# Performance work log

Hardware: AMD Instinct MI355X
Metric: run time of the kernel (lower is better)

## Reference

```python
import jax, jax.numpy as jnp
import numpy as np

N, E, D = 100000, 640000, 128

def setup_inputs() -> dict:
    key = jax.random.key(0)
    ks = jax.random.split(key, 12)
    s = 1.0 / np.sqrt(D)
    sg = 1.0 / np.sqrt(2 * D)
    return {
        "nodes": jax.random.normal(ks[0], (N, D), jnp.float32),
        "globals_": jax.random.normal(ks[1], (1, D), jnp.float32),
        "senders": jax.random.randint(ks[2], (E,), 0, N, jnp.int32),
        "receivers": jax.random.randint(ks[3], (E,), 0, N, jnp.int32),
        "W1_w": jax.random.normal(ks[4], (D, D), jnp.float32) * s,
        "W1_b": jnp.zeros((D,), jnp.float32),
        "W2_w": jax.random.normal(ks[5], (D, D), jnp.float32) * s,
        "W2_b": jnp.zeros((D,), jnp.float32),
        "W3_w": jax.random.normal(ks[6], (D, D), jnp.float32) * s,
        "W3_b": jnp.zeros((D,), jnp.float32),
        "Wg_w": jax.random.normal(ks[7], (2 * D, D), jnp.float32) * sg,
        "Wg_b": jnp.zeros((D,), jnp.float32),
    }


def reference(nodes, globals_, senders, receivers,
              W1_w, W1_b, W2_w, W2_b, W3_w, W3_b, Wg_w, Wg_b):
    n = nodes.shape[0]
    # W1 skip-branch projection
    h = nodes @ W1_w + W1_b                              # [N, D]
    # GraphConvolution: W2 projection + symmetric-normalized sum aggregation
    conv = nodes @ W2_w + W2_b                           # [N, D]
    ones = jnp.ones(senders.shape, conv.dtype)
    send_deg = jax.ops.segment_sum(ones, senders, num_segments=n)
    recv_deg = jax.ops.segment_sum(ones, receivers, num_segments=n)
    conv = conv * jax.lax.rsqrt(jnp.maximum(send_deg, 1.0))[:, None]
    agg = jax.ops.segment_sum(conv[senders], receivers, num_segments=n)  # gather + scatter
    agg = agg * jax.lax.rsqrt(jnp.maximum(recv_deg, 1.0))[:, None]
    h = h + agg
    # global -> node broadcast (globals is not None)
    h = h + (globals_[0:1] @ W3_w + W3_b)
    h = jax.nn.relu(h)
    h = h + nodes                                        # residual
    # global update: aggregate nodes (sum over single graph) + gated residual
    an = jnp.sum(h, axis=0, keepdims=True)               # [1, D]
    g_new = globals_ + jax.nn.relu(jnp.concatenate([an, globals_], axis=-1) @ Wg_w + Wg_b)
    return h, g_new
```

## Files before the change

kernel.cpp:

```cpp
#include <hip/hip_runtime.h>

#define D 128

typedef __attribute__((ext_vector_type(8))) short short8;
typedef __attribute__((ext_vector_type(4))) float floatx4;

__device__ inline void bf16split(float x, ushort& hi, ushort& lo) {
  unsigned u = __float_as_uint(x);
  unsigned rh = (u + 0x7FFFu + ((u >> 16) & 1u)) & 0xFFFF0000u;
  hi = (ushort)(rh >> 16);
  float fl = x - __uint_as_float(rh);
  unsigned ul = __float_as_uint(fl);
  lo = (ushort)((ul + 0x7FFFu + ((ul >> 16) & 1u)) >> 16);
}

__global__ void k_gproj(const float* __restrict__ g, const float* __restrict__ W3,
                        const float* __restrict__ b3, float* __restrict__ gvec) {
  const int j = threadIdx.x;
  float acc = b3[j];
  for (int k = 0; k < D; ++k) acc = fmaf(g[k], W3[k * D + j], acc);
  gvec[j] = acc;
}

__global__ void k_degrees(const int* __restrict__ snd, const int* __restrict__ rcv,
                          int* __restrict__ cs, int* __restrict__ cr, int E) {
  const int e = blockIdx.x * blockDim.x + threadIdx.x;
  if (e < E) {
    atomicAdd(cs + snd[e], 1);
    atomicAdd(cr + rcv[e], 1);
  }
}

__global__ void k_scan(const int* __restrict__ cnt, int* __restrict__ off,
                       int* __restrict__ cursor, int n) {
  __shared__ int part[1024];
  const int t = threadIdx.x;
  int s = 0;
  for (int r = t; r < n; r += 1024) s += cnt[r];
  part[t] = s;
  __syncthreads();
  for (int st = 1; st < 1024; st <<= 1) {
    int v = (t >= st) ? part[t - st] : 0;
    __syncthreads();
    part[t] += v;
    __syncthreads();
  }
  int running = (t == 0) ? 0 : part[t - 1];
  for (int r = t; r < n; r += 1024) {
    off[r] = running;
    cursor[r] = running;
    running += cnt[r];
  }
}

__global__ void k_fill(const int* __restrict__ snd, const int* __restrict__ rcv,
                       int* __restrict__ cursor, int* __restrict__ srt, int E) {
  const int e = blockIdx.x * blockDim.x + threadIdx.x;
  if (e < E) {
    const int p = atomicAdd(cursor + rcv[e], 1);
    srt[p] = snd[e];
  }
}

__global__ void k_wsplit(const float* __restrict__ W1, const float* __restrict__ W2,
                         ushort* __restrict__ wt) {
  const int id = blockIdx.x * blockDim.x + threadIdx.x;
  const int mat = id >> 14;
  const int idx = id & 16383;
  const int k = idx >> 7;
  const int n = idx & 127;
  const float x = (mat ? W2 : W1)[k * D + n];
  ushort hi, lo;
  bf16split(x, hi, lo);
  wt[(size_t)mat * 32768 + (size_t)n * 128 + k] = hi;
  wt[(size_t)mat * 32768 + 16384 + (size_t)n * 128 + k] = lo;
}

__global__ __launch_bounds__(256, 2) void k_dualgemm(
    const float* __restrict__ A, const ushort* __restrict__ wt,
    const float* __restrict__ b1, const float* __restrict__ b2,
    const float* __restrict__ gvec, const int* __restrict__ cnt_send,
    float* __restrict__ outH, float* __restrict__ conv, int n) {
  __shared__ ushort Ah[128 * 64], Al[128 * 64], Wh[128 * 64], Wl[128 * 64];
  const int t = threadIdx.x;
  const int variant = blockIdx.y;
  const int row0 = blockIdx.x * 128;
  const int lane = t & 63, widx = t >> 6;
  const int wr = widx >> 1, wc = widx & 1;
  const int m = lane & 15, quad = lane >> 4;
  const ushort* wtb = wt + (size_t)variant * 32768;

  floatx4 acc[4][4];
#pragma unroll
  for (int i = 0; i < 4; ++i)
#pragma unroll
    for (int j = 0; j < 4; ++j) acc[i][j] = (floatx4)0.f;

  const int srow = t >> 1, shalf = t & 1;

  for (int p = 0; p < 2; ++p) {
    {
      const int grow = row0 + srow;
      const bool ok = grow < n;
      const float* gp = A + (size_t)grow * D + p * 64 + shalf * 32;
#pragma unroll
      for (int c = 0; c < 8; ++c) {
        float4 v = make_float4(0.f, 0.f, 0.f, 0.f);
        if (ok) v = *(const float4*)(gp + 4 * c);
        ushort h0, l0, h1, l1, h2, l2, h3, l3;
        bf16split(v.x, h0, l0); bf16split(v.y, h1, l1);
        bf16split(v.z, h2, l2); bf16split(v.w, h3, l3);
        const int kl = shalf * 32 + 4 * c;
        const int ch = (kl >> 3) ^ (srow & 7);
        const int a = srow * 64 + ch * 8 + (kl & 7);
        *(ushort4*)&Ah[a] = make_ushort4(h0, h1, h2, h3);
        *(ushort4*)&Al[a] = make_ushort4(l0, l1, l2, l3);
      }
    }
    {
      const ushort* gh = wtb + (size_t)srow * 128 + p * 64 + shalf * 32;
      const ushort* gl = gh + 16384;
#pragma unroll
      for (int c = 0; c < 4; ++c) {
        const uint4 vh = *(const uint4*)(gh + 8 * c);
        const uint4 vl = *(const uint4*)(gl + 8 * c);
        const int ch = (shalf * 4 + c) ^ (srow & 7);
        const int a = srow * 64 + ch * 8;
        *(uint4*)&Wh[a] = vh;
        *(uint4*)&Wl[a] = vl;
      }
    }
    __syncthreads();
#pragma unroll
    for (int kk = 0; kk < 2; ++kk) {
      const int swz = (((kk << 2) + quad) ^ (lane & 7)) << 3;
      short8 a_h[4], a_l[4], b_h[4], b_l[4];
#pragma unroll
      for (int i = 0; i < 4; ++i) {
        const int r = (wr * 64 + i * 16 + m) * 64 + swz;
        a_h[i] = *(const short8*)&Ah[r];
        a_l[i] = *(const short8*)&Al[r];
      }
#pragma unroll
      for (int j = 0; j < 4; ++j) {
        const int r = (wc * 64 + j * 16 + m) * 64 + swz;
        b_h[j] = *(const short8*)&Wh[r];
        b_l[j] = *(const short8*)&Wl[r];
      }
#pragma unroll
      for (int i = 0; i < 4; ++i)
#pragma unroll
        for (int j = 0; j < 4; ++j) {
          floatx4 c = acc[i][j];
          c = __builtin_amdgcn_mfma_f32_16x16x32_bf16(a_h[i], b_h[j], c, 0, 0, 0);
          c = __builtin_amdgcn_mfma_f32_16x16x32_bf16(a_h[i], b_l[j], c, 0, 0, 0);
          c = __builtin_amdgcn_mfma_f32_16x16x32_bf16(a_l[i], b_h[j], c, 0, 0, 0);
          acc[i][j] = c;
        }
    }
    __syncthreads();
  }

  if (variant == 0) {
    float bb[4], gg[4];
#pragma unroll
    for (int j = 0; j < 4; ++j) {
      const int col = wc * 64 + j * 16 + m;
      bb[j] = b1[col];
      gg[j] = gvec[col];
    }
#pragma unroll
    for (int i = 0; i < 4; ++i)
#pragma unroll
      for (int pp = 0; pp < 4; ++pp) {
        const int rg = row0 + wr * 64 + i * 16 + quad * 4 + pp;
        if (rg >= n) continue;
#pragma unroll
        for (int j = 0; j < 4; ++j) {
          const int col = wc * 64 + j * 16 + m;
          outH[(size_t)rg * D + col] = acc[i][j][pp] + bb[j] + gg[j];
        }
      }
  } else {
    float bb[4];
#pragma unroll
    for (int j = 0; j < 4; ++j) bb[j] = b2[wc * 64 + j * 16 + m];
#pragma unroll
    for (int i = 0; i < 4; ++i)
#pragma unroll
      for (int pp = 0; pp < 4; ++pp) {
        const int rg = row0 + wr * 64 + i * 16 + quad * 4 + pp;
        if (rg >= n) continue;
        const float sc = rsqrtf(fmaxf((float)cnt_send[rg], 1.f));
#pragma unroll
        for (int j = 0; j < 4; ++j) {
          const int col = wc * 64 + j * 16 + m;
          conv[(size_t)rg * D + col] = (acc[i][j][pp] + bb[j]) * sc;
        }
      }
  }
}

__global__ __launch_bounds__(256) void k_agg_finalize(
    const float* __restrict__ conv, const int* __restrict__ off,
    const int* __restrict__ cnt_recv, const int* __restrict__ srt,
    const float* __restrict__ nodes, float* __restrict__ h,
    float* __restrict__ an, int n) {
  __shared__ float anl[8][D];
  const int hw = threadIdx.x >> 5;
  const int ln = threadIdx.x & 31;
  const int ghw = blockIdx.x * 8 + hw;
  const int nhw = gridDim.x * 8;
  const int c0 = ln * 4;

  float a0 = 0.f, a1 = 0.f, a2 = 0.f, a3 = 0.f;
  for (int r = ghw; r < n; r += nhw) {
    const int dg = cnt_recv[r];
    const int o = off[r];
    const float4 h1 = *(const float4*)(h + (size_t)r * D + c0);
    const float4 nd = *(const float4*)(nodes + (size_t)r * D + c0);
    float sx = 0.f, sy = 0.f, sz = 0.f, sw = 0.f;
    for (int i = 0; i < dg; i += 8) {
      int idx[8];
      float mk[8];
#pragma unroll
      for (int j = 0; j < 8; ++j) {
        const int p = i + j;
        const bool v = p < dg;
        idx[j] = srt[o + (v ? p : 0)];
        mk[j] = v ? 1.f : 0.f;
      }
      float4 c[8];
#pragma unroll
      for (int j = 0; j < 8; ++j)
        c[j] = *(const float4*)(conv + (size_t)idx[j] * D + c0);
#pragma unroll
      for (int j = 0; j < 8; ++j) {
        sx = fmaf(mk[j], c[j].x, sx);
        sy = fmaf(mk[j], c[j].y, sy);
        sz = fmaf(mk[j], c[j].z, sz);
        sw = fmaf(mk[j], c[j].w, sw);
      }
    }
    const float sc = rsqrtf(fmaxf((float)dg, 1.f));
    const float x0 = fmaxf(h1.x + sx * sc, 0.f) + nd.x;
    const float x1 = fmaxf(h1.y + sy * sc, 0.f) + nd.y;
    const float x2 = fmaxf(h1.z + sz * sc, 0.f) + nd.z;
    const float x3 = fmaxf(h1.w + sw * sc, 0.f) + nd.w;
    *(float4*)(h + (size_t)r * D + c0) = make_float4(x0, x1, x2, x3);
    a0 += x0; a1 += x1; a2 += x2; a3 += x3;
  }
  anl[hw][c0 + 0] = a0;
  anl[hw][c0 + 1] = a1;
  anl[hw][c0 + 2] = a2;
  anl[hw][c0 + 3] = a3;
  __syncthreads();
  if (threadIdx.x < D) {
    float s = 0.f;
#pragma unroll
    for (int k = 0; k < 8; ++k) s += anl[k][threadIdx.x];
    atomicAdd(an + threadIdx.x, s);
  }
}

__global__ void k_gupdate(const float* __restrict__ an, const float* __restrict__ g,
                          const float* __restrict__ Wg, const float* __restrict__ bg,
                          float* __restrict__ gout) {
  const int j = threadIdx.x;
  float acc = bg[j];
  for (int k = 0; k < D; ++k) acc = fmaf(an[k], Wg[k * D + j], acc);
  for (int k = 0; k < D; ++k) acc = fmaf(g[k], Wg[(D + k) * D + j], acc);
  gout[j] = g[j] + fmaxf(acc, 0.f);
}

extern "C" void kernel_launch(void* const* d_in, const int* in_sizes, int n_in,
                              void* d_out, int out_size, void* d_ws, size_t ws_size,
                              hipStream_t stream) {
  const float* nodes = (const float*)d_in[0];
  const float* globals_ = (const float*)d_in[1];
  const int* senders = (const int*)d_in[2];
  const int* receivers = (const int*)d_in[3];
  const float* W1_w = (const float*)d_in[4];
  const float* W1_b = (const float*)d_in[5];
  const float* W2_w = (const float*)d_in[6];
  const float* W2_b = (const float*)d_in[7];
  const float* W3_w = (const float*)d_in[8];
  const float* W3_b = (const float*)d_in[9];
  const float* Wg_w = (const float*)d_in[10];
  const float* Wg_b = (const float*)d_in[11];
  const int N = in_sizes[0] / D;
  const int E = in_sizes[2];

  float* h = (float*)d_out;
  float* gout = h + (size_t)N * D;

  float* ws = (float*)d_ws;
  float* conv = ws;
  int* cnt_send = (int*)(ws + (size_t)N * D);
  int* cnt_recv = cnt_send + N;
  int* off = cnt_recv + N;
  int* cursor = off + N;
  int* srt = cursor + N;
  float* gvec = (float*)(srt + E);
  float* an = gvec + D;
  ushort* wt = (ushort*)cursor;

  hipMemsetAsync(cnt_send, 0, 2 * (size_t)N * sizeof(int), stream);
  hipMemsetAsync(an, 0, D * sizeof(float), stream);

  hipLaunchKernelGGL(k_gproj, dim3(1), dim3(D), 0, stream, globals_, W3_w, W3_b, gvec);
  hipLaunchKernelGGL(k_degrees, dim3((E + 255) / 256), dim3(256), 0, stream,
                     senders, receivers, cnt_send, cnt_recv, E);
  hipLaunchKernelGGL(k_scan, dim3(1), dim3(1024), 0, stream, cnt_recv, off, cursor, N);
  hipLaunchKernelGGL(k_fill, dim3((E + 255) / 256), dim3(256), 0, stream,
                     senders, receivers, cursor, srt, E);
  hipLaunchKernelGGL(k_wsplit, dim3(128), dim3(256), 0, stream, W1_w, W2_w, wt);
  hipLaunchKernelGGL(k_dualgemm, dim3((N + 127) / 128, 2), dim3(256), 0, stream,
                     nodes, wt, W1_b, W2_b, gvec, cnt_send, h, conv, N);
  hipLaunchKernelGGL(k_agg_finalize, dim3(2048), dim3(256), 0, stream,
                     conv, off, cnt_recv, srt, nodes, h, an, N);
  hipLaunchKernelGGL(k_gupdate, dim3(1), dim3(D), 0, stream, an, globals_, Wg_w, Wg_b, gout);
}
```

Before: 387.8 us.

## Parallelize scan, fuse dual GEMM into one pass, add nontemporal accesses

Replaces the single-block scan with a three-kernel multi-block scan and merges the two GEMM variants into one kernel. Each 64-row tile now computes both W1 and W2 outputs, so the A tile is loaded and bf16-split once instead of twice. Also adds nontemporal loads and stores in the aggregation kernel, doubles its grid, splits the tiny global GEMVs over 256 threads, and folds the an memset into k_gproj. The GEMM uses a padded LDS layout instead of the XOR swizzle and sets launch bounds to 3 blocks, which may bring bank conflicts or register pressure.

```diff
diff --git a/kernel.cpp b/kernel.cpp
--- a/kernel.cpp
+++ b/kernel.cpp
@@ -1,6 +1,7 @@
 #include <hip/hip_runtime.h>
 
 #define D 128
+#define SCH 1024
 
 typedef __attribute__((ext_vector_type(8))) short short8;
 typedef __attribute__((ext_vector_type(4))) float floatx4;
@@ -14,12 +15,30 @@
   lo = (ushort)((ul + 0x7FFFu + ((ul >> 16) & 1u)) >> 16);
 }
 
+__device__ inline float4 ntload4(const float* p) {
+  floatx4 v = __builtin_nontemporal_load((const floatx4*)p);
+  return make_float4(v.x, v.y, v.z, v.w);
+}
+__device__ inline void ntstore4(float* p, float4 v) {
+  floatx4 u = {v.x, v.y, v.z, v.w};
+  __builtin_nontemporal_store(u, (floatx4*)p);
+}
+
 __global__ void k_gproj(const float* __restrict__ g, const float* __restrict__ W3,
-                        const float* __restrict__ b3, float* __restrict__ gvec) {
-  const int j = threadIdx.x;
-  float acc = b3[j];
-  for (int k = 0; k < D; ++k) acc = fmaf(g[k], W3[k * D + j], acc);
-  gvec[j] = acc;
+                        const float* __restrict__ b3, float* __restrict__ gvec,
+                        float* __restrict__ an) {
+  if (blockIdx.x == 1) {
+    if (threadIdx.x < D) an[threadIdx.x] = 0.f;
+    return;
+  }
+  __shared__ float part[256];
+  const int j = threadIdx.x & 127, half = threadIdx.x >> 7;
+  float acc = 0.f;
+  for (int k = half * 64; k < half * 64 + 64; ++k)
+    acc = fmaf(g[k], W3[k * D + j], acc);
+  part[threadIdx.x] = acc;
+  __syncthreads();
+  if (threadIdx.x < D) gvec[j] = b3[j] + part[j] + part[j + 128];
 }
 
 __global__ void k_degrees(const int* __restrict__ snd, const int* __restrict__ rcv,
@@ -31,25 +50,56 @@
   }
 }
 
-__global__ void k_scan(const int* __restrict__ cnt, int* __restrict__ off,
-                       int* __restrict__ cursor, int n) {
-  __shared__ int part[1024];
+__global__ void k_scanA(const int* __restrict__ cnt, int* __restrict__ bsum, int n) {
+  __shared__ int red[4];
   const int t = threadIdx.x;
-  int s = 0;
-  for (int r = t; r < n; r += 1024) s += cnt[r];
-  part[t] = s;
-  __syncthreads();
-  for (int st = 1; st < 1024; st <<= 1) {
-    int v = (t >= st) ? part[t - st] : 0;
-    __syncthreads();
-    part[t] += v;
-    __syncthreads();
-  }
-  int running = (t == 0) ? 0 : part[t - 1];
-  for (int r = t; r < n; r += 1024) {
-    off[r] = running;
-    cursor[r] = running;
-    running += cnt[r];
+  const int base = blockIdx.x * SCH + t * 4;
+  int4 v = make_int4(0, 0, 0, 0);
+  if (base < n) v = *(const int4*)(cnt + base);
+  int s = v.x + v.y + v.z + v.w;
+#pragma unroll
+  for (int o = 32; o > 0; o >>= 1) s += __shfl_down(s, o, 64);
+  if ((t & 63) == 0) red[t >> 6] = s;
+  __syncthreads();
+  if (t == 0) bsum[blockIdx.x] = red[0] + red[1] + red[2] + red[3];
+}
+
+__global__ void k_scanB(const int* __restrict__ bsum, int* __restrict__ bbase, int nb) {
+  __shared__ int sh[256];
+  const int t = threadIdx.x;
+  const int v = (t < nb) ? bsum[t] : 0;
+  sh[t] = v;
+  __syncthreads();
+  for (int st = 1; st < 256; st <<= 1) {
+    const int u = (t >= st) ? sh[t - st] : 0;
+    __syncthreads();
+    sh[t] += u;
+    __syncthreads();
+  }
+  if (t < nb) bbase[t] = sh[t] - v;
+}
+
+__global__ void k_scanC(const int* __restrict__ cnt, const int* __restrict__ bbase,
+                        int* __restrict__ off, int* __restrict__ cursor, int n) {
+  __shared__ int sh[256];
+  const int t = threadIdx.x;
+  const int base = blockIdx.x * SCH + t * 4;
+  int4 v = make_int4(0, 0, 0, 0);
+  if (base < n) v = *(const int4*)(cnt + base);
+  const int s = v.x + v.y + v.z + v.w;
+  sh[t] = s;
+  __syncthreads();
+  for (int st = 1; st < 256; st <<= 1) {
+    const int u = (t >= st) ? sh[t - st] : 0;
+    __syncthreads();
+    sh[t] += u;
+    __syncthreads();
+  }
+  const int ex = sh[t] - s + bbase[blockIdx.x];
+  if (base < n) {
+    const int4 o = make_int4(ex, ex + v.x, ex + v.x + v.y, ex + v.x + v.y + v.z);
+    *(int4*)(off + base) = o;
+    *(int4*)(cursor + base) = o;
   }
 }
 
@@ -76,19 +126,16 @@
   wt[(size_t)mat * 32768 + 16384 + (size_t)n * 128 + k] = lo;
 }
 
-__global__ __launch_bounds__(256, 2) void k_dualgemm(
+__global__ __launch_bounds__(256, 3) void k_gemm(
     const float* __restrict__ A, const ushort* __restrict__ wt,
     const float* __restrict__ b1, const float* __restrict__ b2,
     const float* __restrict__ gvec, const int* __restrict__ cnt_send,
     float* __restrict__ outH, float* __restrict__ conv, int n) {
-  __shared__ ushort Ah[128 * 64], Al[128 * 64], Wh[128 * 64], Wl[128 * 64];
+  __shared__ ushort Ah[64 * 40], Al[64 * 40], Wh[256 * 40], Wl[256 * 40];
   const int t = threadIdx.x;
-  const int variant = blockIdx.y;
-  const int row0 = blockIdx.x * 128;
-  const int lane = t & 63, widx = t >> 6;
-  const int wr = widx >> 1, wc = widx & 1;
+  const int row0 = blockIdx.x * 64;
+  const int lane = t & 63, w = t >> 6;
   const int m = lane & 15, quad = lane >> 4;
-  const ushort* wtb = wt + (size_t)variant * 32768;
 
   floatx4 acc[4][4];
 #pragma unroll
@@ -96,76 +143,71 @@
 #pragma unroll
     for (int j = 0; j < 4; ++j) acc[i][j] = (floatx4)0.f;
 
-  const int srow = t >> 1, shalf = t & 1;
-
-  for (int p = 0; p < 2; ++p) {
+  const int arow = t >> 2, akl = (t & 3) * 8;
+  const int wcol = t;
+  const int wmat = wcol >> 7, wn = wcol & 127;
+
+  for (int p = 0; p < 4; ++p) {
     {
-      const int grow = row0 + srow;
+      const int grow = row0 + arow;
       const bool ok = grow < n;
-      const float* gp = A + (size_t)grow * D + p * 64 + shalf * 32;
-#pragma unroll
-      for (int c = 0; c < 8; ++c) {
-        float4 v = make_float4(0.f, 0.f, 0.f, 0.f);
-        if (ok) v = *(const float4*)(gp + 4 * c);
-        ushort h0, l0, h1, l1, h2, l2, h3, l3;
-        bf16split(v.x, h0, l0); bf16split(v.y, h1, l1);
-        bf16split(v.z, h2, l2); bf16split(v.w, h3, l3);
-        const int kl = shalf * 32 + 4 * c;
-        const int ch = (kl >> 3) ^ (srow & 7);
-        const int a = srow * 64 + ch * 8 + (kl & 7);
-        *(ushort4*)&Ah[a] = make_ushort4(h0, h1, h2, h3);
-        *(ushort4*)&Al[a] = make_ushort4(l0, l1, l2, l3);
-      }
+      const float* gp = A + (size_t)grow * D + p * 32 + akl;
+      float4 v0 = make_float4(0.f, 0.f, 0.f, 0.f), v1 = v0;
+      if (ok) {
+        v0 = *(const float4*)gp;
+        v1 = *(const float4*)(gp + 4);
+      }
+      ushort h0, l0, h1, l1, h2, l2, h3, l3;
+      const int a = arow * 40 + akl;
+      bf16split(v0.x, h0, l0); bf16split(v0.y, h1, l1);
+      bf16split(v0.z, h2, l2); bf16split(v0.w, h3, l3);
+      *(ushort4*)&Ah[a] = make_ushort4(h0, h1, h2, h3);
+      *(ushort4*)&Al[a] = make_ushort4(l0, l1, l2, l3);
+      bf16split(v1.x, h0, l0); bf16split(v1.y, h1, l1);
+      bf16split(v1.z, h2, l2); bf16split(v1.w, h3, l3);
+      *(ushort4*)&Ah[a + 4] = make_ushort4(h0, h1, h2, h3);
+      *(ushort4*)&Al[a + 4] = make_ushort4(l0, l1, l2, l3);
     }
     {
-      const ushort* gh = wtb + (size_t)srow * 128 + p * 64 + shalf * 32;
+      const ushort* gh = wt + (size_t)wmat * 32768 + (size_t)wn * 128 + p * 32;
       const ushort* gl = gh + 16384;
+      const int a = wcol * 40;
 #pragma unroll
       for (int c = 0; c < 4; ++c) {
-        const uint4 vh = *(const uint4*)(gh + 8 * c);
-        const uint4 vl = *(const uint4*)(gl + 8 * c);
-        const int ch = (shalf * 4 + c) ^ (srow & 7);
-        const int a = srow * 64 + ch * 8;
-        *(uint4*)&Wh[a] = vh;
-        *(uint4*)&Wl[a] = vl;
-      }
-    }
-    __syncthreads();
-#pragma unroll
-    for (int kk = 0; kk < 2; ++kk) {
-      const int swz = (((kk << 2) + quad) ^ (lane & 7)) << 3;
-      short8 a_h[4], a_l[4], b_h[4], b_l[4];
+        *(uint4*)&Wh[a + 8 * c] = *(const uint4*)(gh + 8 * c);
+        *(uint4*)&Wl[a + 8 * c] = *(const uint4*)(gl + 8 * c);
+      }
+    }
+    __syncthreads();
+    short8 a_h[4], a_l[4];
+#pragma unroll
+    for (int i = 0; i < 4; ++i) {
+      const int r = (i * 16 + m) * 40 + quad * 8;
+      a_h[i] = *(const short8*)&Ah[r];
+      a_l[i] = *(const short8*)&Al[r];
+    }
+#pragma unroll
+    for (int j = 0; j < 4; ++j) {
+      const int r = (w * 64 + j * 16 + m) * 40 + quad * 8;
+      const short8 b_h = *(const short8*)&Wh[r];
+      const short8 b_l = *(const short8*)&Wl[r];
 #pragma unroll
       for (int i = 0; i < 4; ++i) {
-        const int r = (wr * 64 + i * 16 + m) * 64 + swz;
-        a_h[i] = *(const short8*)&Ah[r];
-        a_l[i] = *(const short8*)&Al[r];
-      }
-#pragma unroll
-      for (int j = 0; j < 4; ++j) {
-        const int r = (wc * 64 + j * 16 + m) * 64 + swz;
-        b_h[j] = *(const short8*)&Wh[r];
-        b_l[j] = *(const short8*)&Wl[r];
-      }
-#pragma unroll
-      for (int i = 0; i < 4; ++i)
-#pragma unroll
-        for (int j = 0; j < 4; ++j) {
-          floatx4 c = acc[i][j];
-          c = __builtin_amdgcn_mfma_f32_16x16x32_bf16(a_h[i], b_h[j], c, 0, 0, 0);
-          c = __builtin_amdgcn_mfma_f32_16x16x32_bf16(a_h[i], b_l[j], c, 0, 0, 0);
-          c = __builtin_amdgcn_mfma_f32_16x16x32_bf16(a_l[i], b_h[j], c, 0, 0, 0);
-          acc[i][j] = c;
-        }
-    }
-    __syncthreads();
-  }
-
-  if (variant == 0) {
+        floatx4 c = acc[i][j];
+        c = __builtin_amdgcn_mfma_f32_16x16x32_bf16(a_h[i], b_h, c, 0, 0, 0);
+        c = __builtin_amdgcn_mfma_f32_16x16x32_bf16(a_h[i], b_l, c, 0, 0, 0);
+        c = __builtin_amdgcn_mfma_f32_16x16x32_bf16(a_l[i], b_h, c, 0, 0, 0);
+        acc[i][j] = c;
+      }
+    }
+    __syncthreads();
+  }
+
+  if (w < 2) {
     float bb[4], gg[4];
 #pragma unroll
     for (int j = 0; j < 4; ++j) {
-      const int col = wc * 64 + j * 16 + m;
+      const int col = w * 64 + j * 16 + m;
       bb[j] = b1[col];
       gg[j] = gvec[col];
     }
@@ -173,28 +215,28 @@
     for (int i = 0; i < 4; ++i)
 #pragma unroll
       for (int pp = 0; pp < 4; ++pp) {
-        const int rg = row0 + wr * 64 + i * 16 + quad * 4 + pp;
+        const int rg = row0 + i * 16 + quad * 4 + pp;
         if (rg >= n) continue;
 #pragma unroll
         for (int j = 0; j < 4; ++j) {
-          const int col = wc * 64 + j * 16 + m;
+          const int col = w * 64 + j * 16 + m;
           outH[(size_t)rg * D + col] = acc[i][j][pp] + bb[j] + gg[j];
         }
       }
   } else {
     float bb[4];
 #pragma unroll
-    for (int j = 0; j < 4; ++j) bb[j] = b2[wc * 64 + j * 16 + m];
+    for (int j = 0; j < 4; ++j) bb[j] = b2[(w - 2) * 64 + j * 16 + m];
 #pragma unroll
     for (int i = 0; i < 4; ++i)
 #pragma unroll
       for (int pp = 0; pp < 4; ++pp) {
-        const int rg = row0 + wr * 64 + i * 16 + quad * 4 + pp;
+        const int rg = row0 + i * 16 + quad * 4 + pp;
         if (rg >= n) continue;
         const float sc = rsqrtf(fmaxf((float)cnt_send[rg], 1.f));
 #pragma unroll
         for (int j = 0; j < 4; ++j) {
-          const int col = wc * 64 + j * 16 + m;
+          const int col = (w - 2) * 64 + j * 16 + m;
           conv[(size_t)rg * D + col] = (acc[i][j][pp] + bb[j]) * sc;
         }
       }
@@ -217,8 +259,8 @@
   for (int r = ghw; r < n; r += nhw) {
     const int dg = cnt_recv[r];
     const int o = off[r];
-    const float4 h1 = *(const float4*)(h + (size_t)r * D + c0);
-    const float4 nd = *(const float4*)(nodes + (size_t)r * D + c0);
+    const float4 h1 = ntload4(h + (size_t)r * D + c0);
+    const float4 nd = ntload4(nodes + (size_t)r * D + c0);
     float sx = 0.f, sy = 0.f, sz = 0.f, sw = 0.f;
     for (int i = 0; i < dg; i += 8) {
       int idx[8];
@@ -247,7 +289,7 @@
     const float x1 = fmaxf(h1.y + sy * sc, 0.f) + nd.y;
     const float x2 = fmaxf(h1.z + sz * sc, 0.f) + nd.z;
     const float x3 = fmaxf(h1.w + sw * sc, 0.f) + nd.w;
-    *(float4*)(h + (size_t)r * D + c0) = make_float4(x0, x1, x2, x3);
+    ntstore4(h + (size_t)r * D + c0, make_float4(x0, x1, x2, x3));
     a0 += x0; a1 += x1; a2 += x2; a3 += x3;
   }
   anl[hw][c0 + 0] = a0;
@@ -266,11 +308,18 @@
 __global__ void k_gupdate(const float* __restrict__ an, const float* __restrict__ g,
                           const float* __restrict__ Wg, const float* __restrict__ bg,
                           float* __restrict__ gout) {
-  const int j = threadIdx.x;
-  float acc = bg[j];
-  for (int k = 0; k < D; ++k) acc = fmaf(an[k], Wg[k * D + j], acc);
-  for (int k = 0; k < D; ++k) acc = fmaf(g[k], Wg[(D + k) * D + j], acc);
-  gout[j] = g[j] + fmaxf(acc, 0.f);
+  __shared__ float part[256];
+  const int j = threadIdx.x & 127, half = threadIdx.x >> 7;
+  float acc = 0.f;
+  if (half == 0) {
+    for (int k = 0; k < D; ++k) acc = fmaf(an[k], Wg[k * D + j], acc);
+  } else {
+    for (int k = 0; k < D; ++k) acc = fmaf(g[k], Wg[(D + k) * D + j], acc);
+  }
+  part[threadIdx.x] = acc;
+  __syncthreads();
+  if (threadIdx.x < D)
+    gout[j] = g[j] + fmaxf(bg[j] + part[j] + part[j + 128], 0.f);
 }
 
 extern "C" void kernel_launch(void* const* d_in, const int* in_sizes, int n_in,
@@ -290,6 +339,7 @@
   const float* Wg_b = (const float*)d_in[11];
   const int N = in_sizes[0] / D;
   const int E = in_sizes[2];
+  const int nb = (N + SCH - 1) / SCH;
 
   float* h = (float*)d_out;
   float* gout = h + (size_t)N * D;
@@ -303,21 +353,27 @@
   int* srt = cursor + N;
   float* gvec = (float*)(srt + E);
   float* an = gvec + D;
+  int* bsum = (int*)(an + D);
+  int* bbase = bsum + 256;
   ushort* wt = (ushort*)cursor;
 
-  hipMemsetAsync(cnt_send, 0, 2 * (size_t)N * sizeof(int), stream);
-  hipMemsetAsync(an, 0, D * sizeof(float), stream);
-
-  hipLaunchKernelGGL(k_gproj, dim3(1), dim3(D), 0, stream, globals_, W3_w, W3_b, gvec);
+  (void)hipMemsetAsync(cnt_send, 0, 2 * (size_t)N * sizeof(int), stream);
+
+  hipLaunchKernelGGL(k_gproj, dim3(2), dim3(256), 0, stream, globals_, W3_w, W3_b,
+                     gvec, an);
   hipLaunchKernelGGL(k_degrees, dim3((E + 255) / 256), dim3(256), 0, stream,
                      senders, receivers, cnt_send, cnt_recv, E);
-  hipLaunchKernelGGL(k_scan, dim3(1), dim3(1024), 0, stream, cnt_recv, off, cursor, N);
+  hipLaunchKernelGGL(k_scanA, dim3(nb), dim3(256), 0, stream, cnt_recv, bsum, N);
+  hipLaunchKernelGGL(k_scanB, dim3(1), dim3(256), 0, stream, bsum, bbase, nb);
+  hipLaunchKernelGGL(k_scanC, dim3(nb), dim3(256), 0, stream, cnt_recv, bbase,
+                     off, cursor, N);
   hipLaunchKernelGGL(k_fill, dim3((E + 255) / 256), dim3(256), 0, stream,
                      senders, receivers, cursor, srt, E);
   hipLaunchKernelGGL(k_wsplit, dim3(128), dim3(256), 0, stream, W1_w, W2_w, wt);
-  hipLaunchKernelGGL(k_dualgemm, dim3((N + 127) / 128, 2), dim3(256), 0, stream,
+  hipLaunchKernelGGL(k_gemm, dim3((N + 63) / 64), dim3(256), 0, stream,
                      nodes, wt, W1_b, W2_b, gvec, cnt_send, h, conv, N);
-  hipLaunchKernelGGL(k_agg_finalize, dim3(2048), dim3(256), 0, stream,
+  hipLaunchKernelGGL(k_agg_finalize, dim3(4096), dim3(256), 0, stream,
                      conv, off, cnt_recv, srt, nodes, h, an, N);
-  hipLaunchKernelGGL(k_gupdate, dim3(1), dim3(D), 0, stream, an, globals_, Wg_w, Wg_b, gout);
-}
+  hipLaunchKernelGGL(k_gupdate, dim3(1), dim3(256), 0, stream, an, globals_,
+                     Wg_w, Wg_b, gout);
+}
```

New measurement: 395.7 us. 2.1% more time.
